# Kernel optimization log

Measured on AMD Instinct MI355X. Metric: run time of the kernel, lower is better.

## Reference

```python
import jax, jax.numpy as jnp
import numpy as np

B, L, A, F = 4096, 12, 768, 4096  # batch, n_layers, d_activations, d_features


def setup_inputs() -> dict:
    key = jax.random.key(0)
    k_x, k_enc, k_dec, k_m, k_s = jax.random.split(key, 5)
    x = jax.random.normal(k_x, (B, L, A), dtype=jnp.float32)
    # Encoder: uniform(-1/sqrt(F), 1/sqrt(F)) per reset_parameters
    enc_thresh = 1.0 / np.sqrt(F)
    W_enc = jax.random.uniform(k_enc, (L, A, F), jnp.float32, -enc_thresh, enc_thresh)
    # Decoder: triangular weights W_i of shape (i+1, F, A), packed along axis 0.
    # Total rows = L*(L+1)//2. uniform(-1/sqrt(A*L), 1/sqrt(A*L)).
    dec_thresh = 1.0 / np.sqrt(A * L)
    n_tri = L * (L + 1) // 2
    W_dec_packed = jax.random.uniform(k_dec, (n_tri, F, A), jnp.float32, -dec_thresh, dec_thresh)
    # JumpReLU threshold per (layer, feature), init 0.03
    theta = jnp.full((L, F), 0.03, dtype=jnp.float32)
    # Dimensionwise input standardizer stats (per layer, per activation dim)
    in_mean = 0.1 * jax.random.normal(k_m, (L, A), dtype=jnp.float32)
    in_std = 1.0 + 0.1 * jax.random.uniform(k_s, (L, A), dtype=jnp.float32)
    return {"x": x, "in_mean": in_mean, "in_std": in_std, "W_enc": W_enc,
            "theta": theta, "W_dec_packed": W_dec_packed}


def reference(x, in_mean, in_std, W_enc, theta, W_dec_packed):
    # Input standardization: (x - mean) / std, broadcast over batch
    sx = (x - in_mean[None]) / in_std[None]                      # [B, L, A]
    # Encoder: per-layer dense projection
    enc = jnp.einsum('bla,laf->blf', sx, W_enc)                  # [B, L, F]
    # JumpReLU: x * (x > theta)
    act = enc * (enc > theta[None]).astype(enc.dtype)            # [B, L, F]
    # Decoder: triangular accumulation. Layer i reads features of layers 0..i
    # with its own weight tensor W_i (slice of the packed triangular buffer).
    n_layers = W_enc.shape[0]
    preds = []
    off = 0
    for i in range(n_layers):
        W_i = W_dec_packed[off:off + i + 1]                      # [i+1, F, A]
        preds.append(jnp.einsum('blf,lfa->ba', act[:, :i + 1], W_i))
        off += i + 1
    logits = jnp.stack(preds, axis=1)                            # [B, L, A]
    # Original forward returns (logits, encoder_out, concat_w_dec); the
    # concat_w_dec list is just a reshape of the decoder params, omitted here.
    return logits, enc
```

## Files before the change

### kernel.cpp

```cpp
#include <hip/hip_runtime.h>
#include <cstdint>
#include <cstddef>

#define B_ 4096
#define L_ 12
#define A_ 768
#define F_ 4096
#define NTRI 78

typedef __bf16 bf16x8 __attribute__((ext_vector_type(8)));
typedef float f32x4 __attribute__((ext_vector_type(4)));
typedef unsigned short u16x4 __attribute__((ext_vector_type(4)));
typedef unsigned short u16x8 __attribute__((ext_vector_type(8)));

__device__ __forceinline__ unsigned short f32_to_bf16(float f) {
  unsigned int u = __float_as_uint(f);
  u += 0x7fffu + ((u >> 16) & 1u);
  return (unsigned short)(u >> 16);
}

__device__ __forceinline__ void gload_lds16(const void* g, void* l) {
  __builtin_amdgcn_global_load_lds(
      (const __attribute__((address_space(1))) void*)g,
      (__attribute__((address_space(3))) void*)l,
      16, 0, 0);
}

__global__ __launch_bounds__(256) void prep_sx(
    const float* __restrict__ x, const float* __restrict__ mean,
    const float* __restrict__ stdv, unsigned short* __restrict__ sx) {
  size_t i4 = (size_t)blockIdx.x * 256 + threadIdx.x;
  size_t e = i4 * 4;
  if (e >= (size_t)B_ * L_ * A_) return;
  unsigned int a = (unsigned int)(e % A_);
  unsigned int t = (unsigned int)(e / A_);
  unsigned int b = t / L_;
  unsigned int l = t % L_;
  float4 xv = *(const float4*)(x + e);
  float4 mv = *(const float4*)(mean + (size_t)l * A_ + a);
  float4 sv = *(const float4*)(stdv + (size_t)l * A_ + a);
  u16x4 o;
  o.x = f32_to_bf16((xv.x - mv.x) / sv.x);
  o.y = f32_to_bf16((xv.y - mv.y) / sv.y);
  o.z = f32_to_bf16((xv.z - mv.z) / sv.z);
  o.w = f32_to_bf16((xv.w - mv.w) / sv.w);
  *(u16x4*)(sx + ((size_t)l * B_ + b) * A_ + a) = o;
}

__global__ __launch_bounds__(256) void transpose_cvt64(
    const float* __restrict__ in, unsigned short* __restrict__ out,
    int R, int C) {
  __shared__ float tile[64][65];
  const float* inz = in + (size_t)blockIdx.z * R * C;
  unsigned short* outz = out + (size_t)blockIdx.z * R * C;
  const int c0 = blockIdx.x * 64, r0 = blockIdx.y * 64;
  const int t = threadIdx.x;
  {
    const int c = (t & 15) * 4;
    const int rb = t >> 4;
#pragma unroll
    for (int q = 0; q < 4; ++q) {
      const int r = rb + q * 16;
      float4 v = *(const float4*)(inz + (size_t)(r0 + r) * C + (c0 + c));
      tile[r][c] = v.x; tile[r][c + 1] = v.y;
      tile[r][c + 2] = v.z; tile[r][c + 3] = v.w;
    }
  }
  __syncthreads();
  {
    const int c = t >> 2;
    const int rb = (t & 3) * 16;
#pragma unroll
    for (int h = 0; h < 2; ++h) {
      u16x8 o;
#pragma unroll
      for (int j = 0; j < 8; ++j) o[j] = f32_to_bf16(tile[rb + h * 8 + j][c]);
      *(u16x8*)(outz + (size_t)(c0 + c) * R + (r0 + rb + h * 8)) = o;
    }
  }
}

template <class KOffA, class KOffB>
__device__ __forceinline__ void gemm_core64(
    int KT, char* AS, char* BS,
    const char* gA0s, const char* gB0s,
    int ldA, int ldB,
    int w, int wr, int wc, int lane,
    KOffA koffA, KOffB koffB, f32x4 (&acc)[8][4]) {
  const int g = lane >> 4;
  const int fr = lane & 15;
  const uint32_t ssr = (uint32_t)((g ^ ((fr >> 1) & 3)) * 16);
  const uint32_t aBase = (uint32_t)(wr * 128 + fr) * 64 + ssr;
  const uint32_t bBase = (uint32_t)(wc * 64 + fr) * 64 + ssr;

  auto stageA = [&](int kt, int h) {
    const uint32_t off = koffA(kt) + (uint32_t)(h * 64);
    char* d = AS + ((kt & 1) << 15) + (h << 14) + (w << 10);
    gload_lds16(gA0s + off, d);
    gload_lds16(gA0s + off + 128u * (uint32_t)ldA, d + 8192);
  };
  auto stageB = [&](int kt, int h) {
    const uint32_t off = koffB(kt) + (uint32_t)(h * 64);
    char* d = BS + ((kt & 1) << 15) + (h << 14) + (w << 10);
    gload_lds16(gB0s + off, d);
    gload_lds16(gB0s + off + 128u * (uint32_t)ldB, d + 8192);
  };

  stageA(0, 0); stageB(0, 0); stageA(0, 1); stageB(0, 1);
  asm volatile("s_waitcnt vmcnt(4)" ::: "memory");
  __builtin_amdgcn_s_barrier();

  bf16x8 bk[4], aA[4], aB[4];
  for (int kt = 0; kt < KT; ++kt) {
    const char* Ab = AS + ((kt & 1) << 15);
    const char* Bb = BS + ((kt & 1) << 15);
    const bool more = (kt + 1 < KT);
#pragma unroll
    for (int ni = 0; ni < 4; ++ni)
      bk[ni] = *(const bf16x8*)(Bb + bBase + ni * 1024);
#pragma unroll
    for (int mi = 0; mi < 4; ++mi)
      aA[mi] = *(const bf16x8*)(Ab + aBase + mi * 1024);
    if (more) stageA(kt + 1, 0);
    asm volatile("" ::: "memory");
    __builtin_amdgcn_s_barrier();
    __builtin_amdgcn_s_setprio(1);
#pragma unroll
    for (int mi = 0; mi < 4; ++mi)
#pragma unroll
      for (int ni = 0; ni < 4; ++ni)
        acc[mi][ni] = __builtin_amdgcn_mfma_f32_16x16x32_bf16(
            aA[mi], bk[ni], acc[mi][ni], 0, 0, 0);
    __builtin_amdgcn_s_setprio(0);
    asm volatile("" ::: "memory");
    __builtin_amdgcn_s_barrier();
#pragma unroll
    for (int mi = 0; mi < 4; ++mi)
      aB[mi] = *(const bf16x8*)(Ab + aBase + (4 + mi) * 1024);
    if (more) stageB(kt + 1, 0);
    asm volatile("" ::: "memory");
    __builtin_amdgcn_s_barrier();
    __builtin_amdgcn_s_setprio(1);
#pragma unroll
    for (int mi = 0; mi < 4; ++mi)
#pragma unroll
      for (int ni = 0; ni < 4; ++ni)
        acc[mi + 4][ni] = __builtin_amdgcn_mfma_f32_16x16x32_bf16(
            aB[mi], bk[ni], acc[mi + 4][ni], 0, 0, 0);
    __builtin_amdgcn_s_setprio(0);
    if (more) { asm volatile("s_waitcnt vmcnt(4)" ::: "memory"); }
    else      { asm volatile("s_waitcnt vmcnt(0)" ::: "memory"); }
    __builtin_amdgcn_s_barrier();
#pragma unroll
    for (int ni = 0; ni < 4; ++ni)
      bk[ni] = *(const bf16x8*)(Bb + 16384 + bBase + ni * 1024);
#pragma unroll
    for (int mi = 0; mi < 4; ++mi)
      aA[mi] = *(const bf16x8*)(Ab + 16384 + aBase + mi * 1024);
    if (more) stageA(kt + 1, 1);
    asm volatile("" ::: "memory");
    __builtin_amdgcn_s_barrier();
    __builtin_amdgcn_s_setprio(1);
#pragma unroll
    for (int mi = 0; mi < 4; ++mi)
#pragma unroll
      for (int ni = 0; ni < 4; ++ni)
        acc[mi][ni] = __builtin_amdgcn_mfma_f32_16x16x32_bf16(
            aA[mi], bk[ni], acc[mi][ni], 0, 0, 0);
    __builtin_amdgcn_s_setprio(0);
    asm volatile("" ::: "memory");
    __builtin_amdgcn_s_barrier();
#pragma unroll
    for (int mi = 0; mi < 4; ++mi)
      aB[mi] = *(const bf16x8*)(Ab + 16384 + aBase + (4 + mi) * 1024);
    if (more) stageB(kt + 1, 1);
    asm volatile("" ::: "memory");
    __builtin_amdgcn_s_barrier();
    __builtin_amdgcn_s_setprio(1);
#pragma unroll
    for (int mi = 0; mi < 4; ++mi)
#pragma unroll
      for (int ni = 0; ni < 4; ++ni)
        acc[mi + 4][ni] = __builtin_amdgcn_mfma_f32_16x16x32_bf16(
            aB[mi], bk[ni], acc[mi + 4][ni], 0, 0, 0);
    __builtin_amdgcn_s_setprio(0);
    if (more) { asm volatile("s_waitcnt vmcnt(4)" ::: "memory"); }
    __builtin_amdgcn_s_barrier();
  }
}

__global__ __launch_bounds__(512, 2) void enc_fused(
    const unsigned short* __restrict__ sxT,
    const unsigned short* __restrict__ wT,
    const float* __restrict__ theta,
    float* __restrict__ enc_out,
    unsigned short* __restrict__ act,
    const float* __restrict__ wdec_in,
    unsigned short* __restrict__ wdecT_out)
{
  extern __shared__ __align__(16) char lds[];
  const int bidx = blockIdx.x;
  const int grp = bidx / 17;
  const int rem = bidx - grp * 17;

  if (rem >= 8) {
    const int tr = grp * 9 + (rem - 8);
    const int y = tr & 63;
    const int z = 24 + (tr >> 6);
    float (*tile)[65] = (float(*)[65])lds;
    const float* inz = wdec_in + (size_t)z * F_ * A_;
    unsigned short* outz = wdecT_out + (size_t)z * F_ * A_;
    const int r0 = y * 64;
    const int t = threadIdx.x;
    for (int xq = 0; xq < 12; ++xq) {
      const int c0 = xq * 64;
      {
        const int c = (t & 15) * 4;
        const int rb = t >> 4;
#pragma unroll
        for (int q = 0; q < 2; ++q) {
          const int r = rb + q * 32;
          float4 v = *(const float4*)(inz + (size_t)(r0 + r) * A_ + (c0 + c));
          tile[r][c] = v.x; tile[r][c + 1] = v.y;
          tile[r][c + 2] = v.z; tile[r][c + 3] = v.w;
        }
      }
      __syncthreads();
      {
        const int c = t >> 3;
        const int rb8 = (t & 7) * 8;
        u16x8 o;
#pragma unroll
        for (int j = 0; j < 8; ++j) o[j] = f32_to_bf16(tile[rb8 + j][c]);
        *(u16x8*)(outz + (size_t)(c0 + c) * F_ + (r0 + rb8)) = o;
      }
      __syncthreads();
    }
    return;
  }

  char* AS = lds;
  char* BS = lds + 65536;
  const int e = grp * 8 + rem;
  const int wg = (e & 7) * 384 + (e >> 3);
  const int l = wg >> 8;
  const int blk = wg & 255;
  const int m0 = (blk & 15) * 256;
  const int n0 = (blk >> 4) * 256;
  const int tid = threadIdx.x;
  const int w = tid >> 6, lane = tid & 63;
  const int wr = w >> 2, wc = w & 3;
  const int srowS = w * 16 + (lane >> 2);
  const int chnkS = ((lane & 3) ^ ((lane >> 3) & 3)) * 16;

  const char* gA0s = (const char*)sxT +
      ((size_t)l * B_ + m0 + srowS) * (A_ * 2) + chnkS;
  const char* gB0s = (const char*)wT +
      ((size_t)l * F_ + n0 + srowS) * (A_ * 2) + chnkS;

  f32x4 acc[8][4] = {};
  auto koffA = [](int kt) { return (uint32_t)kt * 128u; };
  auto koffB = [](int kt) { return (uint32_t)kt * 128u; };
  gemm_core64(A_ / 64, AS, BS, gA0s, gB0s, A_ * 2, A_ * 2, w, wr, wc, lane,
              koffA, koffB, acc);

  const int g = lane >> 4, fr = lane & 15;
#pragma unroll
  for (int ni = 0; ni < 4; ++ni) {
    const int gcol = n0 + wc * 64 + ni * 16 + fr;
    const float th = theta[(size_t)l * F_ + gcol];
#pragma unroll
    for (int mi = 0; mi < 8; ++mi) {
      const int growb = m0 + wr * 128 + mi * 16 + g * 4;
#pragma unroll
      for (int jj = 0; jj < 4; ++jj) {
        const float v = acc[mi][ni][jj];
        const size_t grow = (size_t)(growb + jj);
        enc_out[(grow * L_ + l) * F_ + gcol] = v;
        act[((size_t)l * B_ + grow) * F_ + gcol] =
            (v > th) ? f32_to_bf16(v) : (unsigned short)0;
      }
    }
  }
}

__global__ __launch_bounds__(512, 2) void dec_gemm8(
    const unsigned short* __restrict__ act,
    const unsigned short* __restrict__ wdecT,
    float* __restrict__ logits)
{
  extern __shared__ __align__(16) char lds[];
  char* AS = lds;
  char* BS = lds + 65536;
  const int b = blockIdx.x;
  const int z = b / 48;
  const int blk = b - z * 48;
  const int i = 11 - z;
  const int m0 = (blk & 15) * 256;
  const int n0 = (blk >> 4) * 256;
  const int triBase = i * (i + 1) / 2;
  const int KT = (i + 1) * 64;
  const int tid = threadIdx.x;
  const int w = tid >> 6, lane = tid & 63;
  const int wr = w >> 2, wc = w & 3;
  const int srowS = w * 16 + (lane >> 2);
  const int chnkS = ((lane & 3) ^ ((lane >> 3) & 3)) * 16;

  const char* gA0s =
      (const char*)act + ((size_t)(m0 + srowS)) * (F_ * 2) + chnkS;
  const char* gB0s = (const char*)wdecT +
      ((size_t)(triBase * A_ + n0 + srowS)) * (F_ * 2) + chnkS;

  f32x4 acc[8][4] = {};
  auto koffA = [](int kt) {
    return (uint32_t)(kt >> 6) * (uint32_t)(B_ * F_ * 2) +
           (uint32_t)(kt & 63) * 128u;
  };
  auto koffB = [](int kt) {
    return (uint32_t)(kt >> 6) * (uint32_t)(A_ * F_ * 2) +
           (uint32_t)(kt & 63) * 128u;
  };
  gemm_core64(KT, AS, BS, gA0s, gB0s, F_ * 2, F_ * 2, w, wr, wc, lane,
              koffA, koffB, acc);

  const int g = lane >> 4, fr = lane & 15;
#pragma unroll
  for (int mi = 0; mi < 8; ++mi) {
    const int growb = m0 + wr * 128 + mi * 16 + g * 4;
#pragma unroll
    for (int ni = 0; ni < 4; ++ni) {
      const int gcol = n0 + wc * 64 + ni * 16 + fr;
#pragma unroll
      for (int jj = 0; jj < 4; ++jj)
        logits[((size_t)(growb + jj) * L_ + i) * A_ + gcol] = acc[mi][ni][jj];
    }
  }
}

extern "C" void kernel_launch(void* const* d_in, const int* in_sizes, int n_in,
                              void* d_out, int out_size, void* d_ws,
                              size_t ws_size, hipStream_t stream) {
  (void)in_sizes; (void)n_in; (void)out_size; (void)ws_size;
  const float* x = (const float*)d_in[0];
  const float* mean = (const float*)d_in[1];
  const float* stdv = (const float*)d_in[2];
  const float* Wenc = (const float*)d_in[3];
  const float* theta = (const float*)d_in[4];
  const float* Wdec = (const float*)d_in[5];

  float* logits = (float*)d_out;
  float* enc = (float*)d_out + (size_t)B_ * L_ * A_;

  char* ws = (char*)d_ws;
  const size_t actBytes = (size_t)L_ * B_ * F_ * 2;
  const size_t sxBytes = (size_t)L_ * B_ * A_ * 2;
  unsigned short* act = (unsigned short*)ws;
  unsigned short* sx = (unsigned short*)(ws + actBytes);
  unsigned short* wencT = (unsigned short*)(ws + actBytes + sxBytes);
  unsigned short* wdecT = (unsigned short*)(ws + actBytes);

  hipFuncSetAttribute((const void*)enc_fused,
                      hipFuncAttributeMaxDynamicSharedMemorySize, 131072);
  hipFuncSetAttribute((const void*)dec_gemm8,
                      hipFuncAttributeMaxDynamicSharedMemorySize, 131072);

  prep_sx<<<(B_ * L_ * A_ / 4 + 255) / 256, 256, 0, stream>>>(x, mean, stdv, sx);
  transpose_cvt64<<<dim3(F_ / 64, A_ / 64, L_), 256, 0, stream>>>(
      Wenc, wencT, A_, F_);
  enc_fused<<<6528, 512, 131072, stream>>>(sx, wencT, theta, enc, act,
                                           Wdec, wdecT);
  transpose_cvt64<<<dim3(A_ / 64, F_ / 64, 24), 256, 0, stream>>>(
      Wdec, wdecT, F_, A_);
  dec_gemm8<<<576, 512, 131072, stream>>>(act, wdecT, logits);
}
```

Measured before the change: 2.757 ms.

## Rewrite decoder GEMM with 12-wave blocks and 4-stage K-pipeline of 32-wide slices

```diff
diff --git a/kernel.cpp b/kernel.cpp
--- a/kernel.cpp
+++ b/kernel.cpp
@@ -284,7 +284,7 @@
   }
 }
 
-__global__ __launch_bounds__(512, 2) void dec_gemm8(
+__global__ __launch_bounds__(768) void dec_gemm12(
     const unsigned short* __restrict__ act,
     const unsigned short* __restrict__ wdecT,
     float* __restrict__ logits)
@@ -293,40 +293,86 @@
   char* AS = lds;
   char* BS = lds + 65536;
   const int b = blockIdx.x;
-  const int z = b / 48;
-  const int blk = b - z * 48;
+  const int z = b >> 6;
+  const int blk = b & 63;
   const int i = 11 - z;
   const int m0 = (blk & 15) * 256;
-  const int n0 = (blk >> 4) * 256;
+  const int n0 = (blk >> 4) * 192;
   const int triBase = i * (i + 1) / 2;
-  const int KT = (i + 1) * 64;
+  const int KT = (i + 1) * 128;
   const int tid = threadIdx.x;
   const int w = tid >> 6, lane = tid & 63;
-  const int wr = w >> 2, wc = w & 3;
-  const int srowS = w * 16 + (lane >> 2);
+  const int wr = w & 3;
+  const int wc = w >> 2;
+  const int g = lane >> 4, fr = lane & 15;
+  const uint32_t ssr = (uint32_t)((g ^ ((fr >> 1) & 3)) * 16);
+  const uint32_t aBase = (uint32_t)(wr * 64 + fr) * 64 + ssr;
+  const uint32_t bBase = (uint32_t)(wc * 64 + fr) * 64 + ssr;
+
+  const bool isA = (w < 8);
   const int chnkS = ((lane & 3) ^ ((lane >> 3) & 3)) * 16;
-
-  const char* gA0s =
-      (const char*)act + ((size_t)(m0 + srowS)) * (F_ * 2) + chnkS;
-  const char* gB0s = (const char*)wdecT +
-      ((size_t)(triBase * A_ + n0 + srowS)) * (F_ * 2) + chnkS;
-
-  f32x4 acc[8][4] = {};
-  auto koffA = [](int kt) {
-    return (uint32_t)(kt >> 6) * (uint32_t)(B_ * F_ * 2) +
-           (uint32_t)(kt & 63) * 128u;
+  const int srowS = isA ? (w * 32 + (lane >> 2))
+                        : ((w - 8) * 48 + (lane >> 2));
+  const char* gS = isA
+      ? (const char*)act + (size_t)(m0 + srowS) * (F_ * 2) + chnkS
+      : (const char*)wdecT +
+            ((size_t)triBase * A_ + n0 + srowS) * (F_ * 2) + chnkS;
+  const size_t layerStride = isA ? (size_t)B_ * F_ * 2 : (size_t)A_ * F_ * 2;
+  char* sBase = isA ? AS : BS;
+  const int slotSz = isA ? 16384 : 12288;
+  const int cOff = isA ? (w << 11) : ((w - 8) * 3072);
+  const int nq = isA ? 2 : 3;
+
+  auto stage = [&](int kt) {
+    const size_t off =
+        (size_t)(kt >> 7) * layerStride + (size_t)((kt & 127) * 64);
+    char* d = sBase + (kt & 3) * slotSz + cOff;
+    for (int q = 0; q < nq; ++q)
+      gload_lds16(gS + off + (size_t)q * (16 * F_ * 2), d + q * 1024);
   };
-  auto koffB = [](int kt) {
-    return (uint32_t)(kt >> 6) * (uint32_t)(A_ * F_ * 2) +
-           (uint32_t)(kt & 63) * 128u;
-  };
-  gemm_core64(KT, AS, BS, gA0s, gB0s, F_ * 2, F_ * 2, w, wr, wc, lane,
-              koffA, koffB, acc);
-
-  const int g = lane >> 4, fr = lane & 15;
-#pragma unroll
-  for (int mi = 0; mi < 8; ++mi) {
-    const int growb = m0 + wr * 128 + mi * 16 + g * 4;
+
+  f32x4 acc[4][4] = {};
+
+  stage(0); stage(1); stage(2);
+  if (isA) { asm volatile("s_waitcnt vmcnt(4)" ::: "memory"); }
+  else     { asm volatile("s_waitcnt vmcnt(6)" ::: "memory"); }
+  __builtin_amdgcn_s_barrier();
+
+  for (int kt = 0; kt < KT; ++kt) {
+    const char* Ab = AS + (kt & 3) * 16384;
+    const char* Bb = BS + (kt & 3) * 12288;
+    bf16x8 ak[4], bk[4];
+#pragma unroll
+    for (int ni = 0; ni < 4; ++ni)
+      bk[ni] = *(const bf16x8*)(Bb + bBase + ni * 1024);
+#pragma unroll
+    for (int mi = 0; mi < 4; ++mi)
+      ak[mi] = *(const bf16x8*)(Ab + aBase + mi * 1024);
+    if (kt + 3 < KT) stage(kt + 3);
+    __builtin_amdgcn_s_setprio(1);
+#pragma unroll
+    for (int mi = 0; mi < 4; ++mi)
+#pragma unroll
+      for (int ni = 0; ni < 4; ++ni)
+        acc[mi][ni] = __builtin_amdgcn_mfma_f32_16x16x32_bf16(
+            ak[mi], bk[ni], acc[mi][ni], 0, 0, 0);
+    __builtin_amdgcn_s_setprio(0);
+    if (kt + 3 < KT) {
+      if (isA) { asm volatile("s_waitcnt vmcnt(4)" ::: "memory"); }
+      else     { asm volatile("s_waitcnt vmcnt(6)" ::: "memory"); }
+    } else if (kt + 2 < KT) {
+      if (isA) { asm volatile("s_waitcnt vmcnt(2)" ::: "memory"); }
+      else     { asm volatile("s_waitcnt vmcnt(3)" ::: "memory"); }
+    } else if (kt + 1 < KT) {
+      asm volatile("s_waitcnt vmcnt(0)" ::: "memory");
+    }
+    asm volatile("" ::: "memory");
+    __builtin_amdgcn_s_barrier();
+  }
+
+#pragma unroll
+  for (int mi = 0; mi < 4; ++mi) {
+    const int growb = m0 + wr * 64 + mi * 16 + g * 4;
 #pragma unroll
     for (int ni = 0; ni < 4; ++ni) {
       const int gcol = n0 + wc * 64 + ni * 16 + fr;
@@ -361,8 +407,8 @@
 
   hipFuncSetAttribute((const void*)enc_fused,
                       hipFuncAttributeMaxDynamicSharedMemorySize, 131072);
-  hipFuncSetAttribute((const void*)dec_gemm8,
-                      hipFuncAttributeMaxDynamicSharedMemorySize, 131072);
+  hipFuncSetAttribute((const void*)dec_gemm12,
+                      hipFuncAttributeMaxDynamicSharedMemorySize, 114688);
 
   prep_sx<<<(B_ * L_ * A_ / 4 + 255) / 256, 256, 0, stream>>>(x, mean, stdv, sx);
   transpose_cvt64<<<dim3(F_ / 64, A_ / 64, L_), 256, 0, stream>>>(
@@ -371,5 +417,5 @@
                                            Wdec, wdecT);
   transpose_cvt64<<<dim3(A_ / 64, F_ / 64, 24), 256, 0, stream>>>(
       Wdec, wdecT, F_, A_);
-  dec_gemm8<<<576, 512, 131072, stream>>>(act, wdecT, logits);
-}
+  dec_gemm12<<<768, 768, 114688, stream>>>(act, wdecT, logits);
+}
```

Measured after the change: 2.945 ms. 6.8% more time.
